# Performance work log

Measured on AMD Instinct MI355X. Metric: run time of the kernel, lower is better.

The kernel has to match this reference:

```python
import jax, jax.numpy as jnp
import numpy as np

N_NODES = 100000
N_EDGES = 600000
DIM = 128
NUM_CLASSES = 10
NUM_GRAPHS = 512
NUM_LAYERS = 4
BN_EPS = 1e-5


def _bn(h, g, b):
    # BatchNorm1d, training-mode statistics (biased variance), affine
    m = h.mean(axis=0)
    v = jnp.var(h, axis=0)
    return (h - m) * jax.lax.rsqrt(v + BN_EPS) * g + b


def setup_inputs() -> dict:
    key = jax.random.key(0)
    ks = jax.random.split(key, 8)
    s_in = 1.0 / np.sqrt(DIM)
    x = jax.random.normal(ks[0], (N_NODES, DIM), dtype=jnp.float32)
    edge_index = jax.random.randint(ks[1], (2, N_EDGES), 0, N_NODES, dtype=jnp.int32)
    batch = jnp.sort(jax.random.randint(ks[2], (N_NODES,), 0, NUM_GRAPHS, dtype=jnp.int32))
    return {
        "x": x,
        "edge_index": edge_index,
        "batch": batch,
        "mlp_w1": jax.random.normal(ks[3], (NUM_LAYERS, DIM, DIM), dtype=jnp.float32) * s_in,
        "mlp_b1": jnp.zeros((NUM_LAYERS, DIM), dtype=jnp.float32),
        "mlp_bn_g": jnp.ones((NUM_LAYERS, DIM), dtype=jnp.float32),
        "mlp_bn_b": jnp.zeros((NUM_LAYERS, DIM), dtype=jnp.float32),
        "mlp_w2": jax.random.normal(ks[4], (NUM_LAYERS, DIM, DIM), dtype=jnp.float32) * s_in,
        "mlp_b2": jnp.zeros((NUM_LAYERS, DIM), dtype=jnp.float32),
        "bn_g": jnp.ones((NUM_LAYERS, DIM), dtype=jnp.float32),
        "bn_b": jnp.zeros((NUM_LAYERS, DIM), dtype=jnp.float32),
        "fc_w": jax.random.normal(ks[5], (NUM_LAYERS + 1, DIM, NUM_CLASSES), dtype=jnp.float32) * s_in,
        "fc_b": jnp.zeros((NUM_LAYERS + 1, NUM_CLASSES), dtype=jnp.float32),
    }


def reference(x, edge_index, batch, mlp_w1, mlp_b1, mlp_bn_g, mlp_bn_b,
              mlp_w2, mlp_b2, bn_g, bn_b, fc_w, fc_b):
    src, dst = edge_index[0], edge_index[1]
    outs = [x]
    h = x
    for i in range(NUM_LAYERS):
        # GINConv: (1+eps)*x + sum_{j in N(i)} x_j  with eps=0 (default)
        agg = jax.ops.segment_sum(h[src], dst, num_segments=N_NODES)
        z = h + agg
        # nn.Sequential(Linear, BatchNorm1d, ReLU, Linear)
        z = jax.nn.relu(_bn(z @ mlp_w1[i] + mlp_b1[i], mlp_bn_g[i], mlp_bn_b[i]))
        z = z @ mlp_w2[i] + mlp_b2[i]
        # outer BN + ReLU
        h = jax.nn.relu(_bn(z, bn_g[i], bn_b[i]))
        outs.append(h)
    out = None
    for i, o in enumerate(outs):
        pooled = jax.ops.segment_sum(o, batch, num_segments=NUM_GRAPHS)
        y = pooled @ fc_w[i] + fc_b[i]  # dropout is identity in eval mode
        out = y if out is None else out + y
    return jax.nn.log_softmax(out, axis=-1)
```

## Files before the change

kernel.cpp:

```cpp
#include <hip/hip_runtime.h>

#define NN 100000
#define NE 600000
#define DD 128
#define NG 512
#define NC 10
#define NL 4

typedef __attribute__((ext_vector_type(8))) short short8;
typedef __attribute__((ext_vector_type(4))) float f32x4;

__device__ __forceinline__ float b2f(unsigned int u) { return __uint_as_float(u << 16); }
__device__ __forceinline__ unsigned int f2b(float f) {
    unsigned int u = __float_as_uint(f);
    return (u + 0x7fffu + ((u >> 16) & 1u)) >> 16;
}
__device__ __forceinline__ void unpack8(uint4 v, float* f) {
    f[0] = b2f(v.x & 0xffffu); f[1] = b2f(v.x >> 16);
    f[2] = b2f(v.y & 0xffffu); f[3] = b2f(v.y >> 16);
    f[4] = b2f(v.z & 0xffffu); f[5] = b2f(v.z >> 16);
    f[6] = b2f(v.w & 0xffffu); f[7] = b2f(v.w >> 16);
}
__device__ __forceinline__ uint4 pack8(const float* f) {
    uint4 v;
    v.x = f2b(f[0]) | (f2b(f[1]) << 16);
    v.y = f2b(f[2]) | (f2b(f[3]) << 16);
    v.z = f2b(f[4]) | (f2b(f[5]) << 16);
    v.w = f2b(f[6]) | (f2b(f[7]) << 16);
    return v;
}

__device__ __forceinline__ void build_bnp(const float* __restrict__ st, const float* __restrict__ gma,
                                          const float* __restrict__ bta, float (*bnp)[DD], int t) {
    if (t < DD) {
        float s = 0.f, q = 0.f;
        #pragma unroll
        for (int r = 0; r < 8; ++r) { s += st[r * DD + t]; q += st[8 * DD + r * DD + t]; }
        const float invn = 1.0f / NN;
        float m = s * invn;
        float var = q * invn - m * m;
        float sc = gma[t] * rsqrtf(var + 1e-5f);
        bnp[0][t] = sc;
        bnp[1][t] = bta[t] - m * sc;
    }
}


__global__ __launch_bounds__(256) void k_zero(float* __restrict__ p, int n) {
    int i = blockIdx.x * 256 + threadIdx.x;
    if (i < n) p[i] = 0.f;
}
__global__ __launch_bounds__(256) void k_zeroint(int* __restrict__ p, int n) {
    int i = blockIdx.x * 256 + threadIdx.x;
    if (i < n) p[i] = 0;
}
__global__ __launch_bounds__(256) void k_copyint(const int* __restrict__ s, int* __restrict__ d, int n) {
    int i = blockIdx.x * 256 + threadIdx.x;
    if (i < n) d[i] = s[i];
}

__global__ __launch_bounds__(256) void k_cvtH(const float* __restrict__ x, ushort* __restrict__ h) {
    int i = blockIdx.x * 256 + threadIdx.x;
    if (i >= NN * DD / 8) return;
    float4 a = ((const float4*)x)[2 * i], b = ((const float4*)x)[2 * i + 1];
    float f[8] = {a.x, a.y, a.z, a.w, b.x, b.y, b.z, b.w};
    ((uint4*)h)[i] = pack8(f);
}

__global__ __launch_bounds__(256) void k_wpack(const float* __restrict__ w1, const float* __restrict__ w2,
                                               ushort* __restrict__ wp) {
    int id = blockIdx.x * 256 + threadIdx.x;
    int v = id & 63;
    int kc = (id >> 6) & 3;
    int ct = (id >> 8) & 7;
    int m = id >> 11;
    const float* W = (m < 4) ? (w1 + (size_t)m * DD * DD) : (w2 + (size_t)(m - 4) * DD * DD);
    int c = ct * 16 + (v & 15);
    int kbase = kc * 32 + ((v >> 4) << 3);
    ushort* dst = wp + ((size_t)id << 3);
    #pragma unroll
    for (int j = 0; j < 8; ++j) dst[j] = (ushort)f2b(W[(size_t)(kbase + j) * DD + c]);
}


__global__ __launch_bounds__(256) void k_hist(const int* __restrict__ dst, int* __restrict__ deg) {
    int e = blockIdx.x * 256 + threadIdx.x;
    if (e < NE) atomicAdd(&deg[dst[e]], 1);
}
__global__ __launch_bounds__(256) void k_partial(const int* __restrict__ deg, int* __restrict__ part) {
    __shared__ int s[256];
    int t = threadIdx.x;
    int i = blockIdx.x * 256 + t;
    s[t] = (i < NN) ? deg[i] : 0;
    __syncthreads();
    #pragma unroll
    for (int off = 128; off >= 1; off >>= 1) {
        if (t < off) s[t] += s[t + off];
        __syncthreads();
    }
    if (t == 0) part[blockIdx.x] = s[0];
}
__global__ __launch_bounds__(512) void k_scanpart(int* __restrict__ part, int nb) {
    __shared__ int s[512];
    int t = threadIdx.x;
    int v = (t < nb) ? part[t] : 0;
    s[t] = v;
    __syncthreads();
    #pragma unroll
    for (int off = 1; off < 512; off <<= 1) {
        int add = (t >= off) ? s[t - off] : 0;
        __syncthreads();
        s[t] += add;
        __syncthreads();
    }
    if (t < nb) part[t] = s[t] - v;
}
__global__ __launch_bounds__(256) void k_exscan(const int* __restrict__ deg, const int* __restrict__ part,
                                                int* __restrict__ rowofs) {
    __shared__ int s[256];
    int b = blockIdx.x, t = threadIdx.x;
    int i = b * 256 + t;
    int v = (i < NN) ? deg[i] : 0;
    s[t] = v;
    __syncthreads();
    #pragma unroll
    for (int off = 1; off < 256; off <<= 1) {
        int add = (t >= off) ? s[t - off] : 0;
        __syncthreads();
        s[t] += add;
        __syncthreads();
    }
    if (i < NN) rowofs[i] = part[b] + s[t] - v;
    if (i == NN - 1) rowofs[NN] = part[b] + s[t];
}
__global__ __launch_bounds__(256) void k_fill(const int* __restrict__ src, const int* __restrict__ dst,
                                              int* __restrict__ cursor, int* __restrict__ csr) {
    int e = blockIdx.x * 256 + threadIdx.x;
    if (e >= NE) return;
    int d = dst[e];
    int pos = atomicAdd(&cursor[d], 1);
    csr[pos] = src[e];
}

template<bool BN>
__global__ __launch_bounds__(256) void k_gather(const int* __restrict__ rowofs, const int* __restrict__ csr,
                                                const ushort* __restrict__ h, ushort* __restrict__ z,
                                                const float* __restrict__ st, const float* __restrict__ gma,
                                                const float* __restrict__ bta) {
    __shared__ float bnp[2][DD];
    int t = threadIdx.x;
    if (BN) {
        build_bnp(st, gma, bta, bnp, t);
        __syncthreads();
    }
    int n = blockIdx.x * 16 + (t >> 4);
    int cl = t & 15;
    int cb = cl * 8;
    float sc[8], sh[8];
    if (BN) {
        #pragma unroll
        for (int j = 0; j < 8; ++j) { sc[j] = bnp[0][cb + j]; sh[j] = bnp[1][cb + j]; }
    }
    float acc[8], f[8];
    uint4 v = ((const uint4*)h)[(size_t)n * 16 + cl];
    unpack8(v, f);
    #pragma unroll
    for (int j = 0; j < 8; ++j)
        acc[j] = BN ? fmaxf(fmaf(f[j], sc[j], sh[j]), 0.f) : f[j];
    int start = rowofs[n], end = rowofs[n + 1];
    for (int e = start; e < end; ++e) {
        int s = csr[e];
        v = ((const uint4*)h)[(size_t)s * 16 + cl];
        unpack8(v, f);
        #pragma unroll
        for (int j = 0; j < 8; ++j)
            acc[j] += BN ? fmaxf(fmaf(f[j], sc[j], sh[j]), 0.f) : f[j];
    }
    ((uint4*)z)[(size_t)n * 16 + cl] = pack8(acc);
}

template<bool TRANS>
__global__ __launch_bounds__(256, 4) void k_mm(const ushort* __restrict__ in, const ushort* __restrict__ wp,
                                               const float* __restrict__ bias,
                                               const float* __restrict__ stin, const float* __restrict__ gma,
                                               const float* __restrict__ bta,
                                               ushort* __restrict__ outp, float* __restrict__ stout) {
    __shared__ __align__(16) char lds[16384];
    __shared__ float bnp[2][DD];
    const int t = threadIdx.x;
    const int lane = t & 63;
    const int wid = t >> 6;
    const int wr = wid >> 1, wc = wid & 1;
    const int rb = blockIdx.x * 64;
    const int rep = blockIdx.x & 7;

    if (TRANS) {
        build_bnp(stin, gma, bta, bnp, t);
        __syncthreads();
    }
    float scv[8], shv[8];
    if (TRANS) {
        int cb = (t & 15) * 8;
        #pragma unroll
        for (int j = 0; j < 8; ++j) { scv[j] = bnp[0][cb + j]; shv[j] = bnp[1][cb + j]; }
    }
    #pragma unroll
    for (int i = 0; i < 4; ++i) {
        int c = i * 256 + t;
        int row = c >> 4;
        int g = rb + row;
        uint4 v = make_uint4(0, 0, 0, 0);
        if (g < NN) {
            v = *((const uint4*)in + (size_t)g * 16 + (c & 15));
            if (TRANS) {
                float f[8];
                unpack8(v, f);
                #pragma unroll
                for (int j = 0; j < 8; ++j) f[j] = fmaxf(fmaf(f[j], scv[j], shv[j]), 0.f);
                v = pack8(f);
            }
        }
        *(uint4*)(lds + ((c * 16) ^ ((row & 7) << 4))) = v;
    }
    __syncthreads();

    f32x4 acc[2][4];
    #pragma unroll
    for (int rt = 0; rt < 2; ++rt)
        #pragma unroll
        for (int ct = 0; ct < 4; ++ct) acc[rt][ct] = (f32x4){0.f, 0.f, 0.f, 0.f};

    #pragma unroll
    for (int kc = 0; kc < 4; ++kc) {
        short8 wf[4];
        #pragma unroll
        for (int ct = 0; ct < 4; ++ct)
            wf[ct] = *(const short8*)(wp + (size_t)((((wc * 4 + ct) * 4 + kc) * 64 + lane) << 3));
        #pragma unroll
        for (int rt = 0; rt < 2; ++rt) {
            int row = wr * 32 + rt * 16 + (lane & 15);
            int off = (row * 256 + ((kc * 32 + ((lane >> 4) << 3)) << 1)) ^ ((row & 7) << 4);
            short8 zf = *(const short8*)(lds + off);
            #pragma unroll
            for (int ct = 0; ct < 4; ++ct)
                acc[rt][ct] = __builtin_amdgcn_mfma_f32_16x16x32_bf16(wf[ct], zf, acc[rt][ct], 0, 0, 0);
        }
    }
    __syncthreads();

    const int zr = lane & 15, cq = lane >> 4;
    #pragma unroll
    for (int rt = 0; rt < 2; ++rt) {
        int row = wr * 32 + rt * 16 + zr;
        #pragma unroll
        for (int ct = 0; ct < 4; ++ct) {
            int c0 = wc * 64 + ct * 16 + cq * 4;
            float4 bi = *(const float4*)(bias + c0);
            f32x4 a = acc[rt][ct];
            uint2 pk;
            pk.x = f2b(a[0] + bi.x) | (f2b(a[1] + bi.y) << 16);
            pk.y = f2b(a[2] + bi.z) | (f2b(a[3] + bi.w) << 16);
            *(uint2*)(lds + ((row * 256 + c0 * 2) ^ ((row & 7) << 4))) = pk;
        }
    }
    __syncthreads();

    float s8[8], q8[8];
    #pragma unroll
    for (int j = 0; j < 8; ++j) { s8[j] = 0.f; q8[j] = 0.f; }
    #pragma unroll
    for (int i = 0; i < 4; ++i) {
        int c = i * 256 + t;
        int row = c >> 4;
        int g = rb + row;
        if (g < NN) {
            uint4 v = *(const uint4*)(lds + ((c * 16) ^ ((row & 7) << 4)));
            ((uint4*)outp)[(size_t)g * 16 + (c & 15)] = v;
            float f[8];
            unpack8(v, f);
            #pragma unroll
            for (int j = 0; j < 8; ++j) { s8[j] += f[j]; q8[j] += f[j] * f[j]; }
        }
    }
    __syncthreads();
    float* rs = (float*)lds;
    float* rq = rs + 16 * DD;
    const int slot = t >> 4, cb2 = (t & 15) * 8;
    #pragma unroll
    for (int j = 0; j < 8; j += 4) {
        *(float4*)(rs + slot * DD + cb2 + j) = make_float4(s8[j], s8[j + 1], s8[j + 2], s8[j + 3]);
        *(float4*)(rq + slot * DD + cb2 + j) = make_float4(q8[j], q8[j + 1], q8[j + 2], q8[j + 3]);
    }
    __syncthreads();
    #pragma unroll
    for (int off = 8; off >= 1; off >>= 1) {
        if (slot < off) {
            #pragma unroll
            for (int j = 0; j < 8; j += 4) {
                float4 a = *(float4*)(rs + slot * DD + cb2 + j);
                float4 b = *(float4*)(rs + (slot + off) * DD + cb2 + j);
                a.x += b.x; a.y += b.y; a.z += b.z; a.w += b.w;
                *(float4*)(rs + slot * DD + cb2 + j) = a;
                float4 c2 = *(float4*)(rq + slot * DD + cb2 + j);
                float4 d  = *(float4*)(rq + (slot + off) * DD + cb2 + j);
                c2.x += d.x; c2.y += d.y; c2.z += d.z; c2.w += d.w;
                *(float4*)(rq + slot * DD + cb2 + j) = c2;
            }
        }
        __syncthreads();
    }
    if (t < DD) {
        atomicAdd(stout + rep * DD + t, rs[t]);
        atomicAdd(stout + 8 * DD + rep * DD + t, rq[t]);
    }
}

__device__ __forceinline__ int lowerb(const int* __restrict__ a, int n, int key) {
    int lo = 0, hi = n;
    while (lo < hi) {
        int mid = (lo + hi) >> 1;
        if (a[mid] < key) lo = mid + 1; else hi = mid;
    }
    return lo;
}

template<bool BN>
__global__ __launch_bounds__(256) void k_pool(const int* __restrict__ batch, const ushort* __restrict__ h,
                                              float* __restrict__ pooled,
                                              const float* __restrict__ st, const float* __restrict__ gma,
                                              const float* __restrict__ bta) {
    __shared__ float bnp[2][DD];
    int t = threadIdx.x;
    if (BN) {
        build_bnp(st, gma, bta, bnp, t);
        __syncthreads();
    }
    int g = blockIdx.x;
    int cl = t & 15;
    int rs = t >> 4;
    int cb = cl * 8;
    float sc[8], sh[8];
    if (BN) {
        #pragma unroll
        for (int j = 0; j < 8; ++j) { sc[j] = bnp[0][cb + j]; sh[j] = bnp[1][cb + j]; }
    }
    int start = lowerb(batch, NN, g);
    int end = lowerb(batch, NN, g + 1);
    float acc[8];
    #pragma unroll
    for (int j = 0; j < 8; ++j) acc[j] = 0.f;
    for (int n = start + rs; n < end; n += 16) {
        uint4 v = ((const uint4*)h)[(size_t)n * 16 + cl];
        float f[8];
        unpack8(v, f);
        #pragma unroll
        for (int j = 0; j < 8; ++j)
            acc[j] += BN ? fmaxf(fmaf(f[j], sc[j], sh[j]), 0.f) : f[j];
    }
    __shared__ float red[16 * DD];
    #pragma unroll
    for (int j = 0; j < 8; j += 4)
        *(float4*)(red + rs * DD + cb + j) = make_float4(acc[j], acc[j + 1], acc[j + 2], acc[j + 3]);
    __syncthreads();
    #pragma unroll
    for (int off = 8; off >= 1; off >>= 1) {
        if (rs < off) {
            #pragma unroll
            for (int j = 0; j < 8; j += 4) {
                float4 a = *(float4*)(red + rs * DD + cb + j);
                float4 b = *(float4*)(red + (rs + off) * DD + cb + j);
                a.x += b.x; a.y += b.y; a.z += b.z; a.w += b.w;
                *(float4*)(red + rs * DD + cb + j) = a;
            }
        }
        __syncthreads();
    }
    if (rs == 0) {
        #pragma unroll
        for (int j = 0; j < 8; j += 4)
            *(float4*)(pooled + (size_t)g * DD + cb + j) = *(float4*)(red + cb + j);
    }
}

__global__ __launch_bounds__(64) void k_readout(const float* __restrict__ pooled, const float* __restrict__ fcw,
                                                const float* __restrict__ fcb, float* __restrict__ out) {
    int g = blockIdx.x, t = threadIdx.x;
    float part[NC];
    #pragma unroll
    for (int c = 0; c < NC; ++c) part[c] = 0.f;
    for (int i = 0; i < NL + 1; ++i) {
        #pragma unroll
        for (int hh = 0; hh < 2; ++hh) {
            int d = t + (hh << 6);
            float v = pooled[((size_t)i * NG + g) * DD + d];
            const float* wr = fcw + ((size_t)i * DD + d) * NC;
            #pragma unroll
            for (int c = 0; c < NC; ++c) part[c] = fmaf(v, wr[c], part[c]);
        }
    }
    #pragma unroll
    for (int off = 32; off >= 1; off >>= 1) {
        #pragma unroll
        for (int c = 0; c < NC; ++c) part[c] += __shfl_down(part[c], off);
    }
    if (t == 0) {
        float y[NC];
        #pragma unroll
        for (int c = 0; c < NC; ++c) {
            float bs = 0.f;
            for (int i = 0; i < NL + 1; ++i) bs += fcb[i * NC + c];
            y[c] = part[c] + bs;
        }
        float m = y[0];
        #pragma unroll
        for (int c = 1; c < NC; ++c) m = fmaxf(m, y[c]);
        float sum = 0.f;
        #pragma unroll
        for (int c = 0; c < NC; ++c) sum += expf(y[c] - m);
        float ls = logf(sum);
        #pragma unroll
        for (int c = 0; c < NC; ++c) out[(size_t)g * NC + c] = y[c] - m - ls;
    }
}


extern "C" void kernel_launch(void* const* d_in, const int* in_sizes, int n_in,
                              void* d_out, int out_size, void* d_ws, size_t ws_size,
                              hipStream_t stream) {
    const float* x   = (const float*)d_in[0];
    const int*   ei  = (const int*)d_in[1];
    const int*   bat = (const int*)d_in[2];
    const float* w1  = (const float*)d_in[3];
    const float* b1  = (const float*)d_in[4];
    const float* mbg = (const float*)d_in[5];
    const float* mbb = (const float*)d_in[6];
    const float* w2  = (const float*)d_in[7];
    const float* b2  = (const float*)d_in[8];
    const float* bng = (const float*)d_in[9];
    const float* bnb = (const float*)d_in[10];
    const float* fcw = (const float*)d_in[11];
    const float* fcb = (const float*)d_in[12];
    float* out = (float*)d_out;

    ushort* H  = (ushort*)d_ws;
    ushort* Z  = H + (size_t)NN * DD;
    ushort* Y1 = Z + (size_t)NN * DD;
    ushort* WP = Y1 + (size_t)NN * DD;
    float* pooled = (float*)(WP + 8 * 16384);
    float* stats  = pooled + (size_t)(NL + 1) * NG * DD;
    int* deg    = (int*)(stats + 8 * 16 * DD);
    int* rowofs = deg + NN;
    int* part   = rowofs + NN + 1;
    int* cursor = part + 512;
    int* csr    = cursor + NN;

    const int* src = ei;
    const int* dst = ei + NE;
    const int nbN = (NN + 255) / 256;
    const int nbE = (NE + 255) / 256;
    const int nstats = 8 * 16 * DD;

    hipLaunchKernelGGL(k_cvtH, dim3(NN * DD / 8 / 256 + 1), dim3(256), 0, stream, x, H);
    hipLaunchKernelGGL(k_zero, dim3((nstats + 255) / 256), dim3(256), 0, stream, stats, nstats);
    hipLaunchKernelGGL(k_zeroint, dim3(nbN), dim3(256), 0, stream, deg, NN);
    hipLaunchKernelGGL(k_hist, dim3(nbE), dim3(256), 0, stream, dst, deg);
    hipLaunchKernelGGL(k_partial, dim3(nbN), dim3(256), 0, stream, deg, part);
    hipLaunchKernelGGL(k_scanpart, dim3(1), dim3(512), 0, stream, part, nbN);
    hipLaunchKernelGGL(k_exscan, dim3(nbN), dim3(256), 0, stream, deg, part, rowofs);
    hipLaunchKernelGGL(k_copyint, dim3(nbN), dim3(256), 0, stream, rowofs, cursor, NN);
    hipLaunchKernelGGL(k_fill, dim3(nbE), dim3(256), 0, stream, src, dst, cursor, csr);
    hipLaunchKernelGGL(k_wpack, dim3(64), dim3(256), 0, stream, w1, w2, WP);

    const int gmm = (NN + 63) / 64;
    const int SLOT = 16 * DD;
    for (int i = 0; i < NL; ++i) {
        float* st_mlp = stats + (size_t)(2 * i + 0) * SLOT;
        float* st_out = stats + (size_t)(2 * i + 1) * SLOT;
        const float* st_prev = stats + (size_t)(2 * i - 1) * SLOT;
        if (i == 0) {
            hipLaunchKernelGGL((k_pool<false>), dim3(NG), dim3(256), 0, stream, bat, H, pooled,
                               (const float*)nullptr, (const float*)nullptr, (const float*)nullptr);
            hipLaunchKernelGGL((k_gather<false>), dim3(NN / 16), dim3(256), 0, stream, rowofs, csr, H, Z,
                               (const float*)nullptr, (const float*)nullptr, (const float*)nullptr);
        } else {
            const float* g = bng + (size_t)(i - 1) * DD;
            const float* b = bnb + (size_t)(i - 1) * DD;
            hipLaunchKernelGGL((k_pool<true>), dim3(NG), dim3(256), 0, stream, bat, H,
                               pooled + (size_t)i * NG * DD, st_prev, g, b);
            hipLaunchKernelGGL((k_gather<true>), dim3(NN / 16), dim3(256), 0, stream, rowofs, csr, H, Z,
                               st_prev, g, b);
        }
        hipLaunchKernelGGL((k_mm<false>), dim3(gmm), dim3(256), 0, stream,
                           Z, WP + (size_t)i * 16384, b1 + (size_t)i * DD,
                           (const float*)nullptr, (const float*)nullptr, (const float*)nullptr,
                           Y1, st_mlp);
        hipLaunchKernelGGL((k_mm<true>), dim3(gmm), dim3(256), 0, stream,
                           Y1, WP + (size_t)(4 + i) * 16384, b2 + (size_t)i * DD,
                           st_mlp, mbg + (size_t)i * DD, mbb + (size_t)i * DD,
                           H, st_out);
    }
    hipLaunchKernelGGL((k_pool<true>), dim3(NG), dim3(256), 0, stream, bat, H,
                       pooled + (size_t)NL * NG * DD,
                       stats + (size_t)7 * SLOT, bng + (size_t)3 * DD, bnb + (size_t)3 * DD);
    hipLaunchKernelGGL(k_readout, dim3(NG), dim3(64), 0, stream, pooled, fcw, fcb, out);
}
```

Baseline: 445.5 us.

## Fuse per-layer pooling into gather and use direct global-to-LDS loads in matmul

```diff
diff --git a/kernel.cpp b/kernel.cpp
--- a/kernel.cpp
+++ b/kernel.cpp
@@ -28,6 +28,11 @@
     v.z = f2b(f[4]) | (f2b(f[5]) << 16);
     v.w = f2b(f[6]) | (f2b(f[7]) << 16);
     return v;
+}
+
+__device__ __forceinline__ void gload_lds16(const void* g, void* l) {
+    __builtin_amdgcn_global_load_lds((__attribute__((address_space(1))) void*)g,
+                                     (__attribute__((address_space(3))) void*)l, 16, 0, 0);
 }
 
 __device__ __forceinline__ void build_bnp(const float* __restrict__ st, const float* __restrict__ gma,
@@ -144,18 +149,22 @@
 
 template<bool BN>
 __global__ __launch_bounds__(256) void k_gather(const int* __restrict__ rowofs, const int* __restrict__ csr,
+                                                const int* __restrict__ batch,
                                                 const ushort* __restrict__ h, ushort* __restrict__ z,
                                                 const float* __restrict__ st, const float* __restrict__ gma,
-                                                const float* __restrict__ bta) {
+                                                const float* __restrict__ bta,
+                                                float* __restrict__ poolslot) {
     __shared__ float bnp[2][DD];
+    __shared__ float sfl[16][DD];
+    __shared__ int gids[16];
     int t = threadIdx.x;
-    if (BN) {
-        build_bnp(st, gma, bta, bnp, t);
-        __syncthreads();
-    }
-    int n = blockIdx.x * 16 + (t >> 4);
+    if (BN) build_bnp(st, gma, bta, bnp, t);
+    int rs = t >> 4;
+    int n = blockIdx.x * 16 + rs;
     int cl = t & 15;
     int cb = cl * 8;
+    if (cl == 0) gids[rs] = batch[n];
+    if (BN) __syncthreads();
     float sc[8], sh[8];
     if (BN) {
         #pragma unroll
@@ -167,14 +176,49 @@
     #pragma unroll
     for (int j = 0; j < 8; ++j)
         acc[j] = BN ? fmaxf(fmaf(f[j], sc[j], sh[j]), 0.f) : f[j];
-    int start = rowofs[n], end = rowofs[n + 1];
-    for (int e = start; e < end; ++e) {
-        int s = csr[e];
-        v = ((const uint4*)h)[(size_t)s * 16 + cl];
-        unpack8(v, f);
+    #pragma unroll
+    for (int j = 0; j < 8; j += 4)
+        *(float4*)(&sfl[rs][cb + j]) = make_float4(acc[j], acc[j + 1], acc[j + 2], acc[j + 3]);
+    __syncthreads();
+    if (t < DD) {
+        float run = sfl[0][t];
+        int gprev = gids[0];
+        #pragma unroll
+        for (int s = 1; s < 16; ++s) {
+            int gg = gids[s];
+            float vv = sfl[s][t];
+            if (gg != gprev) {
+                atomicAdd(poolslot + (size_t)gprev * DD + t, run);
+                run = 0.f;
+                gprev = gg;
+            }
+            run += vv;
+        }
+        atomicAdd(poolslot + (size_t)gprev * DD + t, run);
+    }
+    int e = rowofs[n], end = rowofs[n + 1];
+    for (; e + 1 < end; e += 2) {
+        int s0 = csr[e], s1 = csr[e + 1];
+        uint4 v0 = ((const uint4*)h)[(size_t)s0 * 16 + cl];
+        uint4 v1 = ((const uint4*)h)[(size_t)s1 * 16 + cl];
+        float f0[8], f1[8];
+        unpack8(v0, f0);
+        unpack8(v1, f1);
+        #pragma unroll
+        for (int j = 0; j < 8; ++j) {
+            float a0 = BN ? fmaxf(fmaf(f0[j], sc[j], sh[j]), 0.f) : f0[j];
+            float a1 = BN ? fmaxf(fmaf(f1[j], sc[j], sh[j]), 0.f) : f1[j];
+            acc[j] += a0 + a1;
+        }
+    }
+    if (e < end) {
+        int s0 = csr[e];
+        uint4 v0 = ((const uint4*)h)[(size_t)s0 * 16 + cl];
+        float f0[8];
+        unpack8(v0, f0);
         #pragma unroll
         for (int j = 0; j < 8; ++j)
-            acc[j] += BN ? fmaxf(fmaf(f[j], sc[j], sh[j]), 0.f) : f[j];
+            acc[j] += BN ? fmaxf(fmaf(f0[j], sc[j], sh[j]), 0.f) : f0[j];
     }
     ((uint4*)z)[(size_t)n * 16 + cl] = pack8(acc);
 }
@@ -198,29 +242,39 @@
         build_bnp(stin, gma, bta, bnp, t);
         __syncthreads();
     }
-    float scv[8], shv[8];
-    if (TRANS) {
-        int cb = (t & 15) * 8;
-        #pragma unroll
-        for (int j = 0; j < 8; ++j) { scv[j] = bnp[0][cb + j]; shv[j] = bnp[1][cb + j]; }
-    }
-    #pragma unroll
-    for (int i = 0; i < 4; ++i) {
-        int c = i * 256 + t;
-        int row = c >> 4;
-        int g = rb + row;
-        uint4 v = make_uint4(0, 0, 0, 0);
-        if (g < NN) {
-            v = *((const uint4*)in + (size_t)g * 16 + (c & 15));
-            if (TRANS) {
-                float f[8];
-                unpack8(v, f);
-                #pragma unroll
-                for (int j = 0; j < 8; ++j) f[j] = fmaxf(fmaf(f[j], scv[j], shv[j]), 0.f);
-                v = pack8(f);
+    if (!TRANS && rb + 64 <= NN) {
+        #pragma unroll
+        for (int i = 0; i < 4; ++i) {
+            int p = i * 256 + t;
+            int row = p >> 4;
+            int oc = (p & 15) ^ (row & 7);
+            gload_lds16((const uint4*)in + (size_t)(rb + row) * 16 + oc, lds + p * 16);
+        }
+    } else {
+        float scv[8], shv[8];
+        if (TRANS) {
+            int cb = (t & 15) * 8;
+            #pragma unroll
+            for (int j = 0; j < 8; ++j) { scv[j] = bnp[0][cb + j]; shv[j] = bnp[1][cb + j]; }
+        }
+        #pragma unroll
+        for (int i = 0; i < 4; ++i) {
+            int c = i * 256 + t;
+            int row = c >> 4;
+            int g = rb + row;
+            uint4 v = make_uint4(0, 0, 0, 0);
+            if (g < NN) {
+                v = *((const uint4*)in + (size_t)g * 16 + (c & 15));
+                if (TRANS) {
+                    float f[8];
+                    unpack8(v, f);
+                    #pragma unroll
+                    for (int j = 0; j < 8; ++j) f[j] = fmaxf(fmaf(f[j], scv[j], shv[j]), 0.f);
+                    v = pack8(f);
+                }
             }
-        }
-        *(uint4*)(lds + ((c * 16) ^ ((row & 7) << 4))) = v;
+            *(uint4*)(lds + ((c * 16) ^ ((row & 7) << 4))) = v;
+        }
     }
     __syncthreads();
 
@@ -324,26 +378,21 @@
     return lo;
 }
 
-template<bool BN>
 __global__ __launch_bounds__(256) void k_pool(const int* __restrict__ batch, const ushort* __restrict__ h,
                                               float* __restrict__ pooled,
                                               const float* __restrict__ st, const float* __restrict__ gma,
                                               const float* __restrict__ bta) {
     __shared__ float bnp[2][DD];
     int t = threadIdx.x;
-    if (BN) {
-        build_bnp(st, gma, bta, bnp, t);
-        __syncthreads();
-    }
+    build_bnp(st, gma, bta, bnp, t);
+    __syncthreads();
     int g = blockIdx.x;
     int cl = t & 15;
     int rs = t >> 4;
     int cb = cl * 8;
     float sc[8], sh[8];
-    if (BN) {
-        #pragma unroll
-        for (int j = 0; j < 8; ++j) { sc[j] = bnp[0][cb + j]; sh[j] = bnp[1][cb + j]; }
-    }
+    #pragma unroll
+    for (int j = 0; j < 8; ++j) { sc[j] = bnp[0][cb + j]; sh[j] = bnp[1][cb + j]; }
     int start = lowerb(batch, NN, g);
     int end = lowerb(batch, NN, g + 1);
     float acc[8];
@@ -355,7 +404,7 @@
         unpack8(v, f);
         #pragma unroll
         for (int j = 0; j < 8; ++j)
-            acc[j] += BN ? fmaxf(fmaf(f[j], sc[j], sh[j]), 0.f) : f[j];
+            acc[j] += fmaxf(fmaf(f[j], sc[j], sh[j]), 0.f);
     }
     __shared__ float red[16 * DD];
     #pragma unroll
@@ -458,10 +507,10 @@
     const int* dst = ei + NE;
     const int nbN = (NN + 255) / 256;
     const int nbE = (NE + 255) / 256;
-    const int nstats = 8 * 16 * DD;
+    const int nzero = (NL + 1) * NG * DD + 8 * 16 * DD;
 
     hipLaunchKernelGGL(k_cvtH, dim3(NN * DD / 8 / 256 + 1), dim3(256), 0, stream, x, H);
-    hipLaunchKernelGGL(k_zero, dim3((nstats + 255) / 256), dim3(256), 0, stream, stats, nstats);
+    hipLaunchKernelGGL(k_zero, dim3((nzero + 255) / 256), dim3(256), 0, stream, pooled, nzero);
     hipLaunchKernelGGL(k_zeroint, dim3(nbN), dim3(256), 0, stream, deg, NN);
     hipLaunchKernelGGL(k_hist, dim3(nbE), dim3(256), 0, stream, dst, deg);
     hipLaunchKernelGGL(k_partial, dim3(nbN), dim3(256), 0, stream, deg, part);
@@ -477,18 +526,13 @@
         float* st_mlp = stats + (size_t)(2 * i + 0) * SLOT;
         float* st_out = stats + (size_t)(2 * i + 1) * SLOT;
         const float* st_prev = stats + (size_t)(2 * i - 1) * SLOT;
+        float* poolslot = pooled + (size_t)i * NG * DD;
         if (i == 0) {
-            hipLaunchKernelGGL((k_pool<false>), dim3(NG), dim3(256), 0, stream, bat, H, pooled,
-                               (const float*)nullptr, (const float*)nullptr, (const float*)nullptr);
-            hipLaunchKernelGGL((k_gather<false>), dim3(NN / 16), dim3(256), 0, stream, rowofs, csr, H, Z,
-                               (const float*)nullptr, (const float*)nullptr, (const float*)nullptr);
+            hipLaunchKernelGGL((k_gather<false>), dim3(NN / 16), dim3(256), 0, stream, rowofs, csr, bat, H, Z,
+                               (const float*)nullptr, (const float*)nullptr, (const float*)nullptr, poolslot);
         } else {
-            const float* g = bng + (size_t)(i - 1) * DD;
-            const float* b = bnb + (size_t)(i - 1) * DD;
-            hipLaunchKernelGGL((k_pool<true>), dim3(NG), dim3(256), 0, stream, bat, H,
-                               pooled + (size_t)i * NG * DD, st_prev, g, b);
-            hipLaunchKernelGGL((k_gather<true>), dim3(NN / 16), dim3(256), 0, stream, rowofs, csr, H, Z,
-                               st_prev, g, b);
+            hipLaunchKernelGGL((k_gather<true>), dim3(NN / 16), dim3(256), 0, stream, rowofs, csr, bat, H, Z,
+                               st_prev, bng + (size_t)(i - 1) * DD, bnb + (size_t)(i - 1) * DD, poolslot);
         }
         hipLaunchKernelGGL((k_mm<false>), dim3(gmm), dim3(256), 0, stream,
                            Z, WP + (size_t)i * 16384, b1 + (size_t)i * DD,
@@ -499,7 +543,7 @@
                            st_mlp, mbg + (size_t)i * DD, mbb + (size_t)i * DD,
                            H, st_out);
     }
-    hipLaunchKernelGGL((k_pool<true>), dim3(NG), dim3(256), 0, stream, bat, H,
+    hipLaunchKernelGGL(k_pool, dim3(NG), dim3(256), 0, stream, bat, H,
                        pooled + (size_t)NL * NG * DD,
                        stats + (size_t)7 * SLOT, bng + (size_t)3 * DD, bnb + (size_t)3 * DD);
     hipLaunchKernelGGL(k_readout, dim3(NG), dim3(64), 0, stream, pooled, fcw, fcb, out);
```

After: 381.4 us. -14.4%, faster.
